# Performance work log

Hardware: AMD Instinct MI355X
Metric: run time of the kernel (lower is better)

The kernel has to match this reference:

```python
import jax, jax.numpy as jnp
import numpy as np

B, D, H = 65536, 3, 256  # collocation batch, coord dim, hidden width


def setup_inputs() -> dict:
    key = jax.random.key(0)
    ks = jax.random.split(key, 8)

    def init(k, shape, fan_in):
        return jax.random.normal(k, shape, dtype=jnp.float32) * np.float32(1.0 / np.sqrt(fan_in))

    return {
        "x": jax.random.uniform(ks[0], (B, D), dtype=jnp.float32, minval=0.1, maxval=1.0),
        "W0": init(ks[1], (D, H), D), "b0": jnp.zeros((H,), jnp.float32),
        "W1": init(ks[2], (H, H), H), "b1": jnp.zeros((H,), jnp.float32),
        "W2": init(ks[3], (H, H), H), "b2": jnp.zeros((H,), jnp.float32),
        "W3": init(ks[4], (H, H), H), "b3": jnp.zeros((H,), jnp.float32),
        "Wout": init(ks[5], (H, 1), H), "bout": jnp.zeros((1,), jnp.float32),
    }


def reference(x, W0, b0, W1, b1, W2, b2, W3, b3, Wout, bout):
    # Scalar PINN network u(xi), xi: [D]
    def u_fn(xi):
        h = jnp.tanh(xi @ W0 + b0)
        h = jnp.tanh(h @ W1 + b1)
        h = jnp.tanh(h @ W2 + b2)
        h = jnp.tanh(h @ W3 + b3)
        return (h @ Wout + bout)[0]

    u = jax.vmap(u_fn)(x)                               # [B]
    # batch_gradient: du/dx_i for every coordinate axis (Cartesian: no adjustment)
    grads = jax.vmap(jax.grad(u_fn))(x)                 # [B, D]
    # batch_hessian diagonal: d^2u/dx_i^2 via forward-over-reverse
    hess_fn = jax.jacfwd(jax.grad(u_fn))                # [D, D] per sample
    hess_diag = jax.vmap(lambda xi: jnp.diagonal(hess_fn(xi)))(x)  # [B, D]
    # pack (u, grad, hessian-diagonal) as the PDE-residual ingredients
    return jnp.concatenate([u[:, None], grads, hess_diag], axis=1)  # [B, 1+D+D]
```

## Files before the change

### kernel.cpp

```cpp
#include <hip/hip_runtime.h>
#include <hip/hip_fp16.h>

#define HDIM 256
#define MS 16
#define PAD 8
#define LDAK (HDIM + PAD)

typedef _Float16 half8 __attribute__((ext_vector_type(8)));
typedef float f32x4 __attribute__((ext_vector_type(4)));

__global__ __launch_bounds__(256) void pack_weights(const float* __restrict__ W1,
                                                    const float* __restrict__ W2,
                                                    const float* __restrict__ W3,
                                                    _Float16* __restrict__ out) {
    int tid = blockIdx.x * blockDim.x + threadIdx.x;
    int l = tid >> 16;
    int idx = tid & 65535;
    int k = idx >> 8;
    int n = idx & 255;
    const float* W = (l == 0) ? W1 : (l == 1) ? W2 : W3;
    out[l * 65536 + (((k >> 3) << 8) + n) * 8 + (k & 7)] = (_Float16)W[idx];
}

__global__ __launch_bounds__(256)
void pinn_fused(const float* __restrict__ x,
                const float* __restrict__ W0,
                const float* __restrict__ b0,
                const float* __restrict__ b1,
                const float* __restrict__ b2,
                const float* __restrict__ b3,
                const float* __restrict__ Wout,
                const float* __restrict__ bout,
                const _Float16* __restrict__ Wp,
                float* __restrict__ out) {
    __shared__ __align__(16) _Float16 Abuf[7 * MS][LDAK];
    __shared__ float xs[MS * 3];

    const int tid  = threadIdx.x;
    const int lane = tid & 63;
    const int wid  = tid >> 6;
    const int qd   = lane >> 4;
    const int n15  = lane & 15;
    const int base = blockIdx.x * MS;

    if (tid < MS * 3) xs[tid] = x[base * 3 + tid];
    __syncthreads();

    #pragma unroll
    for (int t = 0; t < 4; ++t) {
        const int n = wid * 64 + t * 16 + n15;
        const float w0 = W0[0 * HDIM + n];
        const float w1 = W0[1 * HDIM + n];
        const float w2 = W0[2 * HDIM + n];
        const float bb = b0[n];
        #pragma unroll
        for (int r = 0; r < 4; ++r) {
            const int m = qd * 4 + r;
            float z  = xs[m*3+0]*w0 + xs[m*3+1]*w1 + xs[m*3+2]*w2 + bb;
            float tv = tanhf(z);
            float dd = 1.f - tv * tv;
            float c2 = -2.f * tv * dd;
            Abuf[0*MS+m][n] = (_Float16)tv;
            Abuf[1*MS+m][n] = (_Float16)(dd * w0);
            Abuf[2*MS+m][n] = (_Float16)(dd * w1);
            Abuf[3*MS+m][n] = (_Float16)(dd * w2);
            Abuf[4*MS+m][n] = (_Float16)(c2 * w0 * w0);
            Abuf[5*MS+m][n] = (_Float16)(c2 * w1 * w1);
            Abuf[6*MS+m][n] = (_Float16)(c2 * w2 * w2);
        }
    }
    __syncthreads();

    #pragma unroll
    for (int l = 0; l < 3; ++l) {
        const _Float16* W = Wp + l * 65536;
        const float* bb = (l == 0) ? b1 : (l == 1) ? b2 : b3;

        f32x4 acc[7][4];
        #pragma unroll
        for (int c = 0; c < 7; ++c)
            #pragma unroll
            for (int t = 0; t < 4; ++t) acc[c][t] = (f32x4){0.f, 0.f, 0.f, 0.f};

        #pragma unroll
        for (int s = 0; s < 8; ++s) {
            half8 bf[4];
            #pragma unroll
            for (int t = 0; t < 4; ++t) {
                const int n = wid * 64 + t * 16 + n15;
                bf[t] = *(const half8*)(W + ((s * 4 + qd) * 256 + n) * 8);
            }
            #pragma unroll
            for (int c = 0; c < 7; ++c) {
                half8 af = *(const half8*)&Abuf[c * MS + n15][s * 32 + qd * 8];
                #pragma unroll
                for (int t = 0; t < 4; ++t)
                    acc[c][t] = __builtin_amdgcn_mfma_f32_16x16x32_f16(af, bf[t], acc[c][t], 0, 0, 0);
            }
        }
        __syncthreads();

        #pragma unroll
        for (int t = 0; t < 4; ++t) {
            const int n = wid * 64 + t * 16 + n15;
            const float bias = bb[n];
            #pragma unroll
            for (int r = 0; r < 4; ++r) {
                const int m = qd * 4 + r;
                float zv = acc[0][t][r] + bias;
                float tv = tanhf(zv);
                float dd = 1.f - tv * tv;
                float c2 = -2.f * tv * dd;
                Abuf[0*MS+m][n] = (_Float16)tv;
                #pragma unroll
                for (int i = 0; i < 3; ++i) {
                    float zg = acc[1 + i][t][r];
                    float zs = acc[4 + i][t][r];
                    Abuf[(1+i)*MS+m][n] = (_Float16)(dd * zg);
                    Abuf[(4+i)*MS+m][n] = (_Float16)(dd * zs + c2 * zg * zg);
                }
            }
        }
        __syncthreads();
    }

    if (tid < 7 * MS) {
        const int c = tid >> 4;
        const int m = tid & 15;
        const _Float16* row = Abuf[tid];
        float accv = 0.f;
        #pragma unroll 4
        for (int k = 0; k < HDIM; k += 8) {
            half8 av = *(const half8*)&row[k];
            #pragma unroll
            for (int j = 0; j < 8; ++j) accv += (float)av[j] * Wout[k + j];
        }
        if (c == 0) accv += bout[0];
        out[(base + m) * 7 + c] = accv;
    }
}

extern "C" void kernel_launch(void* const* d_in, const int* in_sizes, int n_in,
                              void* d_out, int out_size, void* d_ws, size_t ws_size,
                              hipStream_t stream) {
    const float* xp   = (const float*)d_in[0];
    const float* W0   = (const float*)d_in[1];
    const float* b0   = (const float*)d_in[2];
    const float* W1   = (const float*)d_in[3];
    const float* b1   = (const float*)d_in[4];
    const float* W2   = (const float*)d_in[5];
    const float* b2   = (const float*)d_in[6];
    const float* W3   = (const float*)d_in[7];
    const float* b3   = (const float*)d_in[8];
    const float* Wout = (const float*)d_in[9];
    const float* bout = (const float*)d_in[10];
    _Float16* Wp = (_Float16*)d_ws;

    pack_weights<<<768, 256, 0, stream>>>(W1, W2, W3, Wp);
    pinn_fused<<<65536 / MS, 256, 0, stream>>>(xp, W0, b0, b1, b2, b3, Wout, bout, Wp,
                                               (float*)d_out);
}
```

Baseline: 297.2 us.

## Transpose MFMA operands for vectorized LDS stores, fast tanh, split output reduction

Swaps the MFMA A/B operands so each lane owns four consecutive output columns, which lets the tanh epilogue write half4 vectors to LDS instead of scalar halves. Replaces tanhf with an exp plus reciprocal approximation, and vectorizes the layer-0 computation with f32x4 loads of W0 and b0. Also adds a min-blocks-per-SM hint to launch_bounds and splits the final Wout dot product across two threads joined by a shuffle. The approximate tanh reduces accuracy slightly, and the occupancy hint may limit registers for the large accumulator array.

```diff
diff --git a/kernel.cpp b/kernel.cpp
--- a/kernel.cpp
+++ b/kernel.cpp
@@ -7,7 +7,13 @@
 #define LDAK (HDIM + PAD)
 
 typedef _Float16 half8 __attribute__((ext_vector_type(8)));
+typedef _Float16 half4 __attribute__((ext_vector_type(4)));
 typedef float f32x4 __attribute__((ext_vector_type(4)));
+
+__device__ __forceinline__ float fast_tanh(float x) {
+    float e = __expf(2.0f * x);
+    return 1.0f - 2.0f * __builtin_amdgcn_rcpf(e + 1.0f);
+}
 
 __global__ __launch_bounds__(256) void pack_weights(const float* __restrict__ W1,
                                                     const float* __restrict__ W2,
@@ -22,7 +28,7 @@
     out[l * 65536 + (((k >> 3) << 8) + n) * 8 + (k & 7)] = (_Float16)W[idx];
 }
 
-__global__ __launch_bounds__(256)
+__global__ __launch_bounds__(256, 2)
 void pinn_fused(const float* __restrict__ x,
                 const float* __restrict__ W0,
                 const float* __restrict__ b0,
@@ -46,27 +52,35 @@
     if (tid < MS * 3) xs[tid] = x[base * 3 + tid];
     __syncthreads();
 
-    #pragma unroll
-    for (int t = 0; t < 4; ++t) {
-        const int n = wid * 64 + t * 16 + n15;
-        const float w0 = W0[0 * HDIM + n];
-        const float w1 = W0[1 * HDIM + n];
-        const float w2 = W0[2 * HDIM + n];
-        const float bb = b0[n];
+    {
+        const int m = tid & 15;
+        const int n0base = (tid >> 4) * 16;
+        const float x0 = xs[m * 3 + 0], x1 = xs[m * 3 + 1], x2 = xs[m * 3 + 2];
         #pragma unroll
-        for (int r = 0; r < 4; ++r) {
-            const int m = qd * 4 + r;
-            float z  = xs[m*3+0]*w0 + xs[m*3+1]*w1 + xs[m*3+2]*w2 + bb;
-            float tv = tanhf(z);
-            float dd = 1.f - tv * tv;
-            float c2 = -2.f * tv * dd;
-            Abuf[0*MS+m][n] = (_Float16)tv;
-            Abuf[1*MS+m][n] = (_Float16)(dd * w0);
-            Abuf[2*MS+m][n] = (_Float16)(dd * w1);
-            Abuf[3*MS+m][n] = (_Float16)(dd * w2);
-            Abuf[4*MS+m][n] = (_Float16)(c2 * w0 * w0);
-            Abuf[5*MS+m][n] = (_Float16)(c2 * w1 * w1);
-            Abuf[6*MS+m][n] = (_Float16)(c2 * w2 * w2);
+        for (int ch = 0; ch < 4; ++ch) {
+            const int n0 = n0base + ch * 4;
+            f32x4 w0 = *(const f32x4*)(W0 + 0 * HDIM + n0);
+            f32x4 w1 = *(const f32x4*)(W0 + 1 * HDIM + n0);
+            f32x4 w2 = *(const f32x4*)(W0 + 2 * HDIM + n0);
+            f32x4 bv = *(const f32x4*)(b0 + n0);
+            half4 h[7];
+            #pragma unroll
+            for (int r = 0; r < 4; ++r) {
+                float z  = x0 * w0[r] + x1 * w1[r] + x2 * w2[r] + bv[r];
+                float tv = fast_tanh(z);
+                float dd = 1.f - tv * tv;
+                float c2 = -2.f * tv * dd;
+                h[0][r] = (_Float16)tv;
+                h[1][r] = (_Float16)(dd * w0[r]);
+                h[2][r] = (_Float16)(dd * w1[r]);
+                h[3][r] = (_Float16)(dd * w2[r]);
+                h[4][r] = (_Float16)(c2 * w0[r] * w0[r]);
+                h[5][r] = (_Float16)(c2 * w1[r] * w1[r]);
+                h[6][r] = (_Float16)(c2 * w2[r] * w2[r]);
+            }
+            #pragma unroll
+            for (int c = 0; c < 7; ++c)
+                *(half4*)&Abuf[c * MS + m][n0] = h[c];
         }
     }
     __syncthreads();
@@ -84,59 +98,68 @@
 
         #pragma unroll
         for (int s = 0; s < 8; ++s) {
-            half8 bf[4];
+            half8 wf[4];
             #pragma unroll
             for (int t = 0; t < 4; ++t) {
                 const int n = wid * 64 + t * 16 + n15;
-                bf[t] = *(const half8*)(W + ((s * 4 + qd) * 256 + n) * 8);
+                wf[t] = *(const half8*)(W + ((s * 4 + qd) * 256 + n) * 8);
             }
             #pragma unroll
             for (int c = 0; c < 7; ++c) {
                 half8 af = *(const half8*)&Abuf[c * MS + n15][s * 32 + qd * 8];
                 #pragma unroll
                 for (int t = 0; t < 4; ++t)
-                    acc[c][t] = __builtin_amdgcn_mfma_f32_16x16x32_f16(af, bf[t], acc[c][t], 0, 0, 0);
+                    acc[c][t] = __builtin_amdgcn_mfma_f32_16x16x32_f16(wf[t], af, acc[c][t], 0, 0, 0);
             }
         }
         __syncthreads();
 
         #pragma unroll
         for (int t = 0; t < 4; ++t) {
-            const int n = wid * 64 + t * 16 + n15;
-            const float bias = bb[n];
+            const int ncol = wid * 64 + t * 16 + qd * 4;
+            f32x4 bv = *(const f32x4*)(bb + ncol);
+            half4 h[7];
             #pragma unroll
             for (int r = 0; r < 4; ++r) {
-                const int m = qd * 4 + r;
-                float zv = acc[0][t][r] + bias;
-                float tv = tanhf(zv);
+                float zv = acc[0][t][r] + bv[r];
+                float tv = fast_tanh(zv);
                 float dd = 1.f - tv * tv;
                 float c2 = -2.f * tv * dd;
-                Abuf[0*MS+m][n] = (_Float16)tv;
+                h[0][r] = (_Float16)tv;
                 #pragma unroll
                 for (int i = 0; i < 3; ++i) {
                     float zg = acc[1 + i][t][r];
                     float zs = acc[4 + i][t][r];
-                    Abuf[(1+i)*MS+m][n] = (_Float16)(dd * zg);
-                    Abuf[(4+i)*MS+m][n] = (_Float16)(dd * zs + c2 * zg * zg);
+                    h[1 + i][r] = (_Float16)(dd * zg);
+                    h[4 + i][r] = (_Float16)(dd * zs + c2 * zg * zg);
                 }
             }
+            #pragma unroll
+            for (int c = 0; c < 7; ++c)
+                *(half4*)&Abuf[c * MS + n15][ncol] = h[c];
         }
         __syncthreads();
     }
 
-    if (tid < 7 * MS) {
-        const int c = tid >> 4;
-        const int m = tid & 15;
-        const _Float16* row = Abuf[tid];
+    if (tid < 7 * MS * 2) {
+        const int row = tid >> 1;
+        const int h   = tid & 1;
+        const _Float16* rp = &Abuf[row][h * 128];
+        const float* wp = Wout + h * 128;
         float accv = 0.f;
         #pragma unroll 4
-        for (int k = 0; k < HDIM; k += 8) {
-            half8 av = *(const half8*)&row[k];
+        for (int k = 0; k < 128; k += 8) {
+            half8 av = *(const half8*)&rp[k];
             #pragma unroll
-            for (int j = 0; j < 8; ++j) accv += (float)av[j] * Wout[k + j];
+            for (int j = 0; j < 8; ++j) accv += (float)av[j] * wp[k + j];
         }
-        if (c == 0) accv += bout[0];
-        out[(base + m) * 7 + c] = accv;
+        accv += __shfl_xor(accv, 1, 64);
+        if (h == 0) {
+            const int c = row >> 4;
+            const int m = row & 15;
+            if (c == 0) accv += bout[0];
+            out[(base + m) * 7 + c] = accv;
+        }
     }
 }
 
```

Result: faster. 267.8 us (-9.9%).
